# Optimization experiments

Measured on AMD Instinct MI355X. Metric: run time of the kernel, lower is better.

Reference implementation:

```python
import jax, jax.numpy as jnp
import numpy as np

E, R, D, H = 8, 16, 2048, 8192
B, S = 2, 2048
SCALING = 2.0  # lora_alpha / r = 32 / 16


def gelu_new(x):
    # HF ACT2FN['gelu_new'] (tanh approximation), matches Phi config
    c = np.sqrt(2.0 / np.pi).astype(np.float32)
    return 0.5 * x * (1.0 + jnp.tanh(c * (x + 0.044715 * x * x * x)))


def _moe_lora(x, onehot, A, Bm):
    # x: [T,Din], A: [E,R,Din], Bm: [E,Dout,R], onehot: [T,E]
    # per-token low-rank projection for every expert (R is tiny), mask to the
    # assigned expert, then contract (e,r) jointly -> single [T,E*R]@[E*R,Dout] GEMM
    z = jnp.einsum('td,erd->ter', x, A) * onehot[:, :, None]  # [T,E,R]
    return jnp.einsum('ter,ehr->th', z, Bm)                   # [T,Dout]


def setup_inputs() -> dict:
    key = jax.random.key(0)
    ks = jax.random.split(key, 10)
    inv = lambda n: np.float32(1.0 / np.sqrt(n))
    return {
        'hidden_states': jax.random.normal(ks[0], (B, S, D), jnp.float32),
        'expert_idx': jax.random.randint(ks[1], (B, S), 0, E),
        'W1': jax.random.normal(ks[2], (H, D), jnp.float32) * inv(D),
        'b1': jax.random.normal(ks[3], (H,), jnp.float32) * 0.02,
        'A1': jax.random.normal(ks[4], (E, R, D), jnp.float32) * inv(D),
        'B1': jax.random.normal(ks[5], (E, H, R), jnp.float32) * 0.02,
        'W2': jax.random.normal(ks[6], (D, H), jnp.float32) * inv(H),
        'b2': jax.random.normal(ks[7], (D,), jnp.float32) * 0.02,
        'A2': jax.random.normal(ks[8], (E, R, H), jnp.float32) * inv(H),
        'B2': jax.random.normal(ks[9], (E, D, R), jnp.float32) * 0.02,
    }


def reference(hidden_states, expert_idx, W1, b1, A1, B1, W2, b2, A2, B2):
    b, s, d = hidden_states.shape
    x = hidden_states.reshape(b * s, d)                       # [T,D]
    onehot = jax.nn.one_hot(expert_idx.reshape(-1), A1.shape[0], dtype=x.dtype)
    # expert fc1: shared base layer + per-expert LoRA + shared bias
    h1 = x @ W1.T + b1 + SCALING * _moe_lora(x, onehot, A1, B1)
    y = gelu_new(h1)                                          # [T,H]
    # expert fc2
    out = y @ W2.T + b2 + SCALING * _moe_lora(y, onehot, A2, B2)
    return out.reshape(b, s, d)
```

## Files before the change

### kernel.cpp

```cpp
#include <hip/hip_runtime.h>
#include <hip/hip_bf16.h>
#include <math.h>

typedef __bf16 bf16_t;
typedef __bf16 bf16x4_t __attribute__((ext_vector_type(4)));
typedef __bf16 bf16x8_t __attribute__((ext_vector_type(8)));
typedef float  f32x4    __attribute__((ext_vector_type(4)));

#define NE  8
#define NR  16
#define ND  2048
#define NH  8192
#define NT  4096
#define NER 128
#define NK1 (ND + NER)
#define NK2 (NH + NER)

static __device__ __forceinline__ float gelu_fast(float x) {
    const float c2 = 1.5957691216057308f;
    float u2 = c2 * (x + 0.044715f * x * x * x);
    return x / (1.0f + __expf(-u2));
}

static __device__ __forceinline__ void load16_to_lds(const bf16_t* g, bf16_t* l) {
    __builtin_amdgcn_global_load_lds(
        (__attribute__((address_space(1))) void*)(g),
        (__attribute__((address_space(3))) void*)(l),
        16, 0, 0);
}

__global__ __launch_bounds__(256) void conv_x(
    const float* __restrict__ x, bf16_t* __restrict__ Xa1)
{
    const int i  = blockIdx.x * 256 + threadIdx.x;
    const int row = i >> 9;
    const int c4  = i & 511;
    f32x4 v = *(const f32x4*)(x + (long)i * 4);
    bf16x4_t o = {(bf16_t)v[0], (bf16_t)v[1], (bf16_t)v[2], (bf16_t)v[3]};
    *(bf16x4_t*)(Xa1 + (long)row * NK1 + (c4 << 2)) = o;
}

__global__ __launch_bounds__(256) void prep_main(
    const float* __restrict__ W, bf16_t* __restrict__ Waug,
    int ld, int shift, int total4)
{
    const int i = blockIdx.x * 256 + threadIdx.x;
    if (i >= total4) return;
    const int row = i >> shift;
    const int c4  = i & ((1 << shift) - 1);
    f32x4 v = *(const f32x4*)(W + (long)i * 4);
    bf16x4_t o = {(bf16_t)v[0], (bf16_t)v[1], (bf16_t)v[2], (bf16_t)v[3]};
    *(bf16x4_t*)(Waug + (long)row * ld + (c4 << 2)) = o;
}

__global__ __launch_bounds__(256) void prep_lora(
    const float* __restrict__ Bl, bf16_t* __restrict__ Waug,
    int nrows, int K0, int ld, int total)
{
    const int i = blockIdx.x * 256 + threadIdx.x;
    if (i >= total) return;
    const int row = i >> 7;
    const int c   = i & 127;
    const int e   = c >> 4;
    const int r   = c & 15;
    float v = Bl[((long)e * nrows + row) * NR + r];
    Waug[(long)row * ld + K0 + c] = (bf16_t)v;
}

template <int SPLITS, int LD>
__global__ __launch_bounds__(256) void zred(
    const float* __restrict__ zp, const int* __restrict__ eidx,
    bf16_t* __restrict__ dst)
{
    const int i = blockIdx.x * 256 + threadIdx.x;
    const int t = i >> 7;
    const int c = i & 127;
    float s = 0.f;
#pragma unroll
    for (int j = 0; j < SPLITS; ++j) s += zp[(long)j * NT * 128 + i];
    const int e = eidx[t];
    float v = ((c >> 4) == e) ? 2.0f * s : 0.f;
    dst[(long)t * LD + c] = (bf16_t)v;
}

template <int K, int LDA, int LDB, int LDC, int MODE>
__global__ __launch_bounds__(256) void gemm_bt(
    const bf16_t* __restrict__ A,  const bf16_t* __restrict__ Bt,
    const float* __restrict__ bias, void* __restrict__ Cout)
{
    __shared__ union {
        struct { bf16_t As[128 * 64]; bf16_t Bs[128 * 64]; } s;
        bf16_t Cs[64 * 136];
    } u;

    const int tid   = threadIdx.x;
    const int wave  = tid >> 6;
    const int lane  = tid & 63;
    const int col16 = lane & 15;
    const int q     = lane >> 4;
    const int wm    = wave & 1;
    const int wn    = wave >> 1;

    const int  rowA0 = blockIdx.y * 128;
    const int  colB0 = (MODE == 3) ? 0 : blockIdx.x * 128;
    const long koff  = (MODE == 3) ? (long)blockIdx.x * K : 0;

    const int srow  = lane >> 3;
    const int skoff = (lane & 7) * 8;

    const bf16_t* Ag = A  + (long)(rowA0 + wave * 32 + srow) * LDA + koff + skoff;
    const bf16_t* Bg = Bt + (long)(colB0 + wave * 32 + srow) * LDB + koff + skoff;
    bf16_t* AsD = &u.s.As[wave * 32 * 64];
    bf16_t* BsD = &u.s.Bs[wave * 32 * 64];

    const bf16_t* Ard = &u.s.As[(wm * 64 + col16) * 64 + q * 8];
    const bf16_t* Brd = &u.s.Bs[(wn * 64 + col16) * 64 + q * 8];

    f32x4 acc[4][4];
#pragma unroll
    for (int i = 0; i < 4; ++i)
#pragma unroll
        for (int j = 0; j < 4; ++j)
            acc[i][j] = (f32x4){0.f, 0.f, 0.f, 0.f};

    for (int it = 0; it < K / 64; ++it) {
#pragma unroll
        for (int j = 0; j < 4; ++j) {
            load16_to_lds(Ag + (long)(j * 8) * LDA, AsD + j * 8 * 64);
            load16_to_lds(Bg + (long)(j * 8) * LDB, BsD + j * 8 * 64);
        }
        Ag += 64; Bg += 64;
        __syncthreads();

#pragma unroll
        for (int h = 0; h < 2; ++h) {
            bf16x8_t af[4], bfr[4];
#pragma unroll
            for (int mt = 0; mt < 4; ++mt)
                af[mt] = *(const bf16x8_t*)(Ard + mt * 16 * 64 + h * 32);
#pragma unroll
            for (int nt = 0; nt < 4; ++nt)
                bfr[nt] = *(const bf16x8_t*)(Brd + nt * 16 * 64 + h * 32);
#pragma unroll
            for (int mt = 0; mt < 4; ++mt)
#pragma unroll
                for (int nt = 0; nt < 4; ++nt)
                    acc[mt][nt] = __builtin_amdgcn_mfma_f32_16x16x32_bf16(
                        af[mt], bfr[nt], acc[mt][nt], 0, 0, 0);
        }
        __syncthreads();
    }

    if (MODE == 1) {
        float* Cf = (float*)Cout;
#pragma unroll
        for (int nt = 0; nt < 4; ++nt) {
            const int col = colB0 + wn * 64 + nt * 16 + col16;
            const float bv = bias[col];
#pragma unroll
            for (int mt = 0; mt < 4; ++mt) {
                const int row0 = rowA0 + wm * 64 + mt * 16 + q * 4;
#pragma unroll
                for (int i = 0; i < 4; ++i)
                    Cf[(long)(row0 + i) * LDC + col] = acc[mt][nt][i] + bv;
            }
        }
    } else if (MODE == 3) {
        float* Cf = (float*)Cout + (long)blockIdx.x * NT * LDC;
#pragma unroll
        for (int nt = 0; nt < 4; ++nt) {
            const int col = wn * 64 + nt * 16 + col16;
#pragma unroll
            for (int mt = 0; mt < 4; ++mt) {
                const int row0 = rowA0 + wm * 64 + mt * 16 + q * 4;
#pragma unroll
                for (int i = 0; i < 4; ++i)
                    Cf[(long)(row0 + i) * LDC + col] = acc[mt][nt][i];
            }
        }
    } else {
        bf16_t* Cb = (bf16_t*)Cout;
#pragma unroll
        for (int half = 0; half < 2; ++half) {
            if (wm == half) {
#pragma unroll
                for (int nt = 0; nt < 4; ++nt) {
                    const int c = wn * 64 + nt * 16 + col16;
                    const float bv = bias[colB0 + c];
#pragma unroll
                    for (int mt = 0; mt < 4; ++mt) {
                        const int rl = mt * 16 + q * 4;
#pragma unroll
                        for (int i = 0; i < 4; ++i)
                            u.Cs[(rl + i) * 136 + c] =
                                (bf16_t)gelu_fast(acc[mt][nt][i] + bv);
                    }
                }
            }
            __syncthreads();
            {
                const int r  = tid >> 2;
                const int c0 = (tid & 3) * 32;
                const long gbase =
                    (long)(rowA0 + half * 64 + r) * LDC + colB0 + c0;
#pragma unroll
                for (int ch = 0; ch < 4; ++ch) {
                    bf16x8_t v = *(const bf16x8_t*)&u.Cs[r * 136 + c0 + ch * 8];
                    *(bf16x8_t*)&Cb[gbase + ch * 8] = v;
                }
            }
            __syncthreads();
        }
    }
}

extern "C" void kernel_launch(void* const* d_in, const int* in_sizes, int n_in,
                              void* d_out, int out_size, void* d_ws, size_t ws_size,
                              hipStream_t stream)
{
    const float* x    = (const float*)d_in[0];
    const int*   eidx = (const int*)  d_in[1];
    const float* W1   = (const float*)d_in[2];
    const float* b1   = (const float*)d_in[3];
    const float* A1   = (const float*)d_in[4];
    const float* B1   = (const float*)d_in[5];
    const float* W2   = (const float*)d_in[6];
    const float* b2   = (const float*)d_in[7];
    const float* A2   = (const float*)d_in[8];
    const float* B2   = (const float*)d_in[9];
    float* out = (float*)d_out;

    char* ws = (char*)d_ws;
    bf16_t* Xaug2 = (bf16_t*)(ws);
    bf16_t* Xaug1 = (bf16_t*)(ws + 68157440L);
    bf16_t* W1aug = (bf16_t*)(ws + 85983232L);
    bf16_t* W2aug = (bf16_t*)(ws + 68157440L);
    bf16_t* A1b   = (bf16_t*)(ws + 104000000L);
    bf16_t* A2b   = (bf16_t*)(ws + 104857600L);
    float*  zp1   = (float*) (ws + 106954752L);
    float*  zp2   = (float*) (ws + 85983232L);

    conv_x<<<NT * ND / 4 / 256, 256, 0, stream>>>(x, Xaug1);
    prep_main<<<(NER * ND / 4) / 256, 256, 0, stream>>>(A1, A1b, ND, 9, NER * ND / 4);
    {
        dim3 g(4, NT / 128);
        gemm_bt<512, NK1, ND, 128, 3><<<g, 256, 0, stream>>>(
            Xaug1, A1b, nullptr, (void*)zp1);
    }
    zred<4, NK1><<<NT * 128 / 256, 256, 0, stream>>>(zp1, eidx, Xaug1 + ND);
    prep_main<<<(NH * ND / 4) / 256, 256, 0, stream>>>(W1, W1aug, NK1, 9, NH * ND / 4);
    prep_lora<<<(NH * NER) / 256, 256, 0, stream>>>(B1, W1aug, NH, ND, NK1, NH * NER);
    {
        dim3 g(NH / 128, NT / 128);
        gemm_bt<NK1, NK1, NK1, NK2, 0><<<g, 256, 0, stream>>>(
            Xaug1, W1aug, b1, (void*)Xaug2);
    }

    prep_main<<<(NER * NH / 4) / 256, 256, 0, stream>>>(A2, A2b, NH, 11, NER * NH / 4);
    {
        dim3 g(8, NT / 128);
        gemm_bt<1024, NK2, NH, 128, 3><<<g, 256, 0, stream>>>(
            Xaug2, A2b, nullptr, (void*)zp2);
    }
    zred<8, NK2><<<NT * 128 / 256, 256, 0, stream>>>(zp2, eidx, Xaug2 + NH);
    prep_main<<<(ND * NH / 4) / 256, 256, 0, stream>>>(W2, W2aug, NK2, 11, ND * NH / 4);
    prep_lora<<<(ND * NER) / 256, 256, 0, stream>>>(B2, W2aug, ND, NH, NK2, ND * NER);
    {
        dim3 g(ND / 128, NT / 128);
        gemm_bt<NK2, NK2, NK2, ND, 1><<<g, 256, 0, stream>>>(
            Xaug2, W2aug, b2, (void*)out);
    }
}
```

Baseline: 658.0 us.

## Split LDS tiles into k-halves, swizzle block order, widen conversion kernels

```diff
diff --git a/kernel.cpp b/kernel.cpp
--- a/kernel.cpp
+++ b/kernel.cpp
@@ -33,24 +33,28 @@
     const float* __restrict__ x, bf16_t* __restrict__ Xa1)
 {
     const int i  = blockIdx.x * 256 + threadIdx.x;
-    const int row = i >> 9;
-    const int c4  = i & 511;
-    f32x4 v = *(const f32x4*)(x + (long)i * 4);
-    bf16x4_t o = {(bf16_t)v[0], (bf16_t)v[1], (bf16_t)v[2], (bf16_t)v[3]};
-    *(bf16x4_t*)(Xa1 + (long)row * NK1 + (c4 << 2)) = o;
+    const int row = i >> 8;
+    const int c8  = i & 255;
+    f32x4 v0 = *(const f32x4*)(x + (long)i * 8);
+    f32x4 v1 = *(const f32x4*)(x + (long)i * 8 + 4);
+    bf16x8_t o = {(bf16_t)v0[0], (bf16_t)v0[1], (bf16_t)v0[2], (bf16_t)v0[3],
+                  (bf16_t)v1[0], (bf16_t)v1[1], (bf16_t)v1[2], (bf16_t)v1[3]};
+    *(bf16x8_t*)(Xa1 + (long)row * NK1 + (c8 << 3)) = o;
 }
 
 __global__ __launch_bounds__(256) void prep_main(
     const float* __restrict__ W, bf16_t* __restrict__ Waug,
-    int ld, int shift, int total4)
+    int ld, int shift8, int total8)
 {
     const int i = blockIdx.x * 256 + threadIdx.x;
-    if (i >= total4) return;
-    const int row = i >> shift;
-    const int c4  = i & ((1 << shift) - 1);
-    f32x4 v = *(const f32x4*)(W + (long)i * 4);
-    bf16x4_t o = {(bf16_t)v[0], (bf16_t)v[1], (bf16_t)v[2], (bf16_t)v[3]};
-    *(bf16x4_t*)(Waug + (long)row * ld + (c4 << 2)) = o;
+    if (i >= total8) return;
+    const int row = i >> shift8;
+    const int c8  = i & ((1 << shift8) - 1);
+    f32x4 v0 = *(const f32x4*)(W + (long)i * 8);
+    f32x4 v1 = *(const f32x4*)(W + (long)i * 8 + 4);
+    bf16x8_t o = {(bf16_t)v0[0], (bf16_t)v0[1], (bf16_t)v0[2], (bf16_t)v0[3],
+                  (bf16_t)v1[0], (bf16_t)v1[1], (bf16_t)v1[2], (bf16_t)v1[3]};
+    *(bf16x8_t*)(Waug + (long)row * ld + (c8 << 3)) = o;
 }
 
 __global__ __launch_bounds__(256) void prep_lora(
@@ -83,13 +87,13 @@
     dst[(long)t * LD + c] = (bf16_t)v;
 }
 
-template <int K, int LDA, int LDB, int LDC, int MODE>
+template <int K, int LDA, int LDB, int LDC, int MODE, int GX>
 __global__ __launch_bounds__(256) void gemm_bt(
     const bf16_t* __restrict__ A,  const bf16_t* __restrict__ Bt,
     const float* __restrict__ bias, void* __restrict__ Cout)
 {
     __shared__ union {
-        struct { bf16_t As[128 * 64]; bf16_t Bs[128 * 64]; } s;
+        struct { bf16_t As[2 * 128 * 32]; bf16_t Bs[2 * 128 * 32]; } s;
         bf16_t Cs[64 * 136];
     } u;
 
@@ -101,20 +105,32 @@
     const int wm    = wave & 1;
     const int wn    = wave >> 1;
 
-    const int  rowA0 = blockIdx.y * 128;
-    const int  colB0 = (MODE == 3) ? 0 : blockIdx.x * 128;
-    const long koff  = (MODE == 3) ? (long)blockIdx.x * K : 0;
-
-    const int srow  = lane >> 3;
-    const int skoff = (lane & 7) * 8;
+    int rowA0, colB0;
+    long koff = 0;
+    if (MODE == 3) {
+        rowA0 = blockIdx.y * 128;
+        colB0 = 0;
+        koff  = (long)blockIdx.x * K;
+    } else {
+        const int lin = blockIdx.y * GX + blockIdx.x;
+        const int PG  = 8 * GX;
+        const int gid = lin / PG;
+        const int pm  = (gid << 3) + (lin & 7);
+        const int pn  = (lin & (PG - 1)) >> 3;
+        rowA0 = pm * 128;
+        colB0 = pn * 128;
+    }
+
+    const int srow  = lane >> 2;
+    const int skoff = (lane & 3) * 8;
 
     const bf16_t* Ag = A  + (long)(rowA0 + wave * 32 + srow) * LDA + koff + skoff;
     const bf16_t* Bg = Bt + (long)(colB0 + wave * 32 + srow) * LDB + koff + skoff;
-    bf16_t* AsD = &u.s.As[wave * 32 * 64];
-    bf16_t* BsD = &u.s.Bs[wave * 32 * 64];
-
-    const bf16_t* Ard = &u.s.As[(wm * 64 + col16) * 64 + q * 8];
-    const bf16_t* Brd = &u.s.Bs[(wn * 64 + col16) * 64 + q * 8];
+    bf16_t* AsD = &u.s.As[wave * 32 * 32];
+    bf16_t* BsD = &u.s.Bs[wave * 32 * 32];
+
+    const bf16_t* Ard = &u.s.As[(wm * 64 + col16) * 32 + q * 8];
+    const bf16_t* Brd = &u.s.Bs[(wn * 64 + col16) * 32 + q * 8];
 
     f32x4 acc[4][4];
 #pragma unroll
@@ -125,9 +141,14 @@
 
     for (int it = 0; it < K / 64; ++it) {
 #pragma unroll
-        for (int j = 0; j < 4; ++j) {
-            load16_to_lds(Ag + (long)(j * 8) * LDA, AsD + j * 8 * 64);
-            load16_to_lds(Bg + (long)(j * 8) * LDB, BsD + j * 8 * 64);
+        for (int h = 0; h < 2; ++h) {
+#pragma unroll
+            for (int j = 0; j < 2; ++j) {
+                load16_to_lds(Ag + h * 32 + (long)(j * 16) * LDA,
+                              AsD + h * 128 * 32 + j * 16 * 32);
+                load16_to_lds(Bg + h * 32 + (long)(j * 16) * LDB,
+                              BsD + h * 128 * 32 + j * 16 * 32);
+            }
         }
         Ag += 64; Bg += 64;
         __syncthreads();
@@ -137,10 +158,10 @@
             bf16x8_t af[4], bfr[4];
 #pragma unroll
             for (int mt = 0; mt < 4; ++mt)
-                af[mt] = *(const bf16x8_t*)(Ard + mt * 16 * 64 + h * 32);
+                af[mt] = *(const bf16x8_t*)(Ard + h * 4096 + mt * 16 * 32);
 #pragma unroll
             for (int nt = 0; nt < 4; ++nt)
-                bfr[nt] = *(const bf16x8_t*)(Brd + nt * 16 * 64 + h * 32);
+                bfr[nt] = *(const bf16x8_t*)(Brd + h * 4096 + nt * 16 * 32);
 #pragma unroll
             for (int mt = 0; mt < 4; ++mt)
 #pragma unroll
@@ -240,34 +261,34 @@
     float*  zp1   = (float*) (ws + 106954752L);
     float*  zp2   = (float*) (ws + 85983232L);
 
-    conv_x<<<NT * ND / 4 / 256, 256, 0, stream>>>(x, Xaug1);
-    prep_main<<<(NER * ND / 4) / 256, 256, 0, stream>>>(A1, A1b, ND, 9, NER * ND / 4);
+    conv_x<<<NT * ND / 8 / 256, 256, 0, stream>>>(x, Xaug1);
+    prep_main<<<(NER * ND / 8) / 256, 256, 0, stream>>>(A1, A1b, ND, 8, NER * ND / 8);
     {
         dim3 g(4, NT / 128);
-        gemm_bt<512, NK1, ND, 128, 3><<<g, 256, 0, stream>>>(
+        gemm_bt<512, NK1, ND, 128, 3, 4><<<g, 256, 0, stream>>>(
             Xaug1, A1b, nullptr, (void*)zp1);
     }
     zred<4, NK1><<<NT * 128 / 256, 256, 0, stream>>>(zp1, eidx, Xaug1 + ND);
-    prep_main<<<(NH * ND / 4) / 256, 256, 0, stream>>>(W1, W1aug, NK1, 9, NH * ND / 4);
+    prep_main<<<(NH * ND / 8) / 256, 256, 0, stream>>>(W1, W1aug, NK1, 8, NH * ND / 8);
     prep_lora<<<(NH * NER) / 256, 256, 0, stream>>>(B1, W1aug, NH, ND, NK1, NH * NER);
     {
         dim3 g(NH / 128, NT / 128);
-        gemm_bt<NK1, NK1, NK1, NK2, 0><<<g, 256, 0, stream>>>(
+        gemm_bt<NK1, NK1, NK1, NK2, 0, NH / 128><<<g, 256, 0, stream>>>(
             Xaug1, W1aug, b1, (void*)Xaug2);
     }
 
-    prep_main<<<(NER * NH / 4) / 256, 256, 0, stream>>>(A2, A2b, NH, 11, NER * NH / 4);
+    prep_main<<<(NER * NH / 8) / 256, 256, 0, stream>>>(A2, A2b, NH, 10, NER * NH / 8);
     {
         dim3 g(8, NT / 128);
-        gemm_bt<1024, NK2, NH, 128, 3><<<g, 256, 0, stream>>>(
+        gemm_bt<1024, NK2, NH, 128, 3, 8><<<g, 256, 0, stream>>>(
             Xaug2, A2b, nullptr, (void*)zp2);
     }
     zred<8, NK2><<<NT * 128 / 256, 256, 0, stream>>>(zp2, eidx, Xaug2 + NH);
-    prep_main<<<(ND * NH / 4) / 256, 256, 0, stream>>>(W2, W2aug, NK2, 11, ND * NH / 4);
+    prep_main<<<(ND * NH / 8) / 256, 256, 0, stream>>>(W2, W2aug, NK2, 10, ND * NH / 8);
     prep_lora<<<(ND * NER) / 256, 256, 0, stream>>>(B2, W2aug, ND, NH, NK2, ND * NER);
     {
         dim3 g(ND / 128, NT / 128);
-        gemm_bt<NK2, NK2, NK2, ND, 1><<<g, 256, 0, stream>>>(
+        gemm_bt<NK2, NK2, NK2, ND, 1, ND / 128><<<g, 256, 0, stream>>>(
             Xaug2, W2aug, b2, (void*)out);
     }
 }
```

Result: faster. 615.9 us (-6.4%).
